# Performance work log

Measured on AMD Instinct MI355X. Metric: run time of the kernel, lower is better.

The kernel has to match this reference:

```python
import jax, jax.numpy as jnp
import numpy as np

B, T = 8, 32
D = 256                      # recurrent dim = 4*8*8 (product of embed dims)
SPEAKERS = 2
OUT_CELL = 64
N_CLASSES = 6
NUM_LAYERS = 2               # original shares ONE QRNNCell across layers ([cell]*num_layers)
BETA = 0.8                   # QActivation beta (scale_factor = 1)

def _unitary(rng, n):
    a = rng.normal(size=(n, n)) + 1j * rng.normal(size=(n, n))
    q, _ = np.linalg.qr(a)
    return jnp.asarray(q.real, jnp.float32), jnp.asarray(q.imag, jnp.float32)

def setup_inputs():
    key = jax.random.key(0)
    ks = jax.random.split(key, 18)
    rng = np.random.default_rng(0)
    def lin(k, fi, fo):
        kw, kb = jax.random.split(k)
        lim = 1.0 / np.sqrt(fi)
        return (jax.random.uniform(kw, (fi, fo), jnp.float32, -lim, lim),
                jax.random.uniform(kb, (fo,), jnp.float32, -lim, lim))
    Wt, bt = lin(ks[0], 300, 4)
    Wa, ba = lin(ks[1], 74, 8)
    Wv, bv = lin(ks[2], 35, 8)
    W1, b1 = lin(ks[3], D, OUT_CELL)
    W2, b2 = lin(ks[4], OUT_CELL, N_CLASSES)
    Ux_r, Ux_i = _unitary(rng, D)
    Uh_r, Uh_i = _unitary(rng, D)
    two_pi = float(2.0 * np.pi)
    return {
        'x_text': jax.random.normal(ks[5], (B, T, 300), jnp.float32),
        'x_audio': jax.random.normal(ks[6], (B, T, 74), jnp.float32),
        'x_video': jax.random.normal(ks[7], (B, T, 35), jnp.float32),
        'smask': jax.random.uniform(ks[8], (B, T, SPEAKERS), jnp.float32),
        'Wt': Wt, 'bt': bt, 'Wa': Wa, 'ba': ba, 'Wv': Wv, 'bv': bv,
        'Pt': jax.random.uniform(ks[9], (SPEAKERS, 4), jnp.float32, 0.0, two_pi),
        'Pa': jax.random.uniform(ks[10], (SPEAKERS, 8), jnp.float32, 0.0, two_pi),
        'Pv': jax.random.uniform(ks[11], (SPEAKERS, 8), jnp.float32, 0.0, two_pi),
        'Ux_r': Ux_r, 'Ux_i': Ux_i, 'Uh_r': Uh_r, 'Uh_i': Uh_i,
        'Lambda': jax.random.normal(ks[12], (), jnp.float32),
        'Kr': jax.random.normal(ks[13], (D, D), jnp.float32),
        'Ki': jax.random.normal(ks[14], (D, D), jnp.float32),
        'W1': W1, 'b1': b1, 'W2': W2, 'b2': b2,
    }

def _forward(x_text, x_audio, x_video, spk, Wt, bt, Wa, ba, Wv, bv, Pt, Pa, Pv,
             Ux_r, Ux_i, Uh_r, Uh_i, Lambda, Kr, Ki, W1, b1, W2, b2):
    def pure_state(x, W, b, P):
        r = jax.nn.relu(x @ W + b)
        amp = r / jnp.maximum(jnp.linalg.norm(r, axis=-1, keepdims=True), 1e-12)  # F.normalize
        ph = P[spk]                                   # (B,T,e) phase lookup by speaker id
        return amp * jnp.cos(ph), amp * jnp.sin(ph)   # ComplexMultiply
    tr_, ti_ = pure_state(x_text, Wt, bt, Pt)
    ar_, ai_ = pure_state(x_audio, Wa, ba, Pa)
    vr_, vi_ = pure_state(x_video, Wv, bv, Pv)
    def ckron(xr, xi, yr, yi):                        # QProduct: complex Kronecker product
        rr = jnp.einsum('bti,btj->btij', xr, yr) - jnp.einsum('bti,btj->btij', xi, yi)
        ii = jnp.einsum('bti,btj->btij', xr, yi) + jnp.einsum('bti,btj->btij', xi, yr)
        b_, t_ = rr.shape[:2]
        return rr.reshape(b_, t_, -1), ii.reshape(b_, t_, -1)
    pr, pi = ckron(tr_, ti_, ar_, ai_)
    pr, pi = ckron(pr, pi, vr_, vi_)                  # (B,T,D)
    # QOuter: rho = |psi><psi|, stored time-major for the scan
    rho_r = jnp.einsum('bti,btj->tbij', pr, pr) + jnp.einsum('bti,btj->tbij', pi, pi)
    rho_i = jnp.einsum('bti,btj->tbij', pi, pr) - jnp.einsum('bti,btj->tbij', pr, pi)
    lam = jax.nn.sigmoid(Lambda)
    eye = jnp.eye(D, dtype=pr.dtype) / D
    def evolve(Ur, Ui, rr, ri):                       # U rho U^dagger (complex, real/imag parts)
        Ar = jnp.einsum('pq,bqr->bpr', Ur, rr) - jnp.einsum('pq,bqr->bpr', Ui, ri)
        Ai = jnp.einsum('pq,bqr->bpr', Ur, ri) + jnp.einsum('pq,bqr->bpr', Ui, rr)
        Br = jnp.einsum('bpq,rq->bpr', Ar, Ur) + jnp.einsum('bpq,rq->bpr', Ai, Ui)
        Bi = jnp.einsum('bpq,rq->bpr', Ai, Ur) - jnp.einsum('bpq,rq->bpr', Ar, Ui)
        return Br, Bi
    def step(carry, x):                               # QRNNCell; activation only on emitted state
        hr, hi = carry
        xr, xi = x
        xer, xei = evolve(Ux_r, Ux_i, xr, xi)
        her, hei = evolve(Uh_r, Uh_i, hr, hi)
        nr = lam * xer + (1.0 - lam) * her
        ni = lam * xei + (1.0 - lam) * hei
        return (nr, ni), (BETA * nr + (1.0 - BETA) * eye, BETA * ni)  # QActivation (depolarize)
    xs = (rho_r, rho_i)
    for _ in range(NUM_LAYERS):                       # same (shared) cell each layer
        init = (jnp.broadcast_to(eye, rho_r.shape[1:]), jnp.zeros(rho_r.shape[1:], pr.dtype))
        _, xs = jax.lax.scan(step, init, xs)
    hr, hi = xs                                       # (T,B,D,D)
    # QMeasurement: p_k = Re <v_k| rho |v_k>, v_k L2-normalized complex vectors
    nrm = jnp.sqrt(jnp.sum(Kr * Kr + Ki * Ki, axis=-1, keepdims=True))
    mr, mi = Kr / nrm, Ki / nrm
    Prj_r = jnp.einsum('ki,kj->kij', mr, mr) + jnp.einsum('ki,kj->kij', mi, mi)
    Prj_i = jnp.einsum('ki,kj->kij', mr, mi) - jnp.einsum('ki,kj->kij', mi, mr)
    probs = jnp.einsum('tbij,kij->tbk', hr, Prj_r) - jnp.einsum('tbij,kij->tbk', hi, Prj_i)
    h1 = jax.nn.relu(probs @ W1 + b1)                 # SimpleNet (dropout = identity at eval)
    out = jnp.tanh(h1 @ W2 + b2)                      # (T,B,C)
    return jax.nn.log_softmax(jnp.moveaxis(out, 0, 1), axis=-1)  # (B,T,C)

def reference(x_text, x_audio, x_video, smask, Wt, bt, Wa, ba, Wv, bv, Pt, Pa, Pv,
              Ux_r, Ux_i, Uh_r, Uh_i, Lambda, Kr, Ki, W1, b1, W2, b2):
    spk = jnp.argmax(smask, axis=-1)
    return _forward(x_text, x_audio, x_video, spk, Wt, bt, Wa, ba, Wv, bv, Pt, Pa, Pv,
                    Ux_r, Ux_i, Uh_r, Uh_i, Lambda, Kr, Ki, W1, b1, W2, b2)
```

## Files before the change

### kernel.cpp

```cpp
#include <hip/hip_runtime.h>

#define TT 32
#define BETA_ 0.8f

typedef __bf16 bf16_t;
typedef bf16_t bf16x8 __attribute__((ext_vector_type(8)));
typedef float f32x4 __attribute__((ext_vector_type(4)));

#define PACC_F 256
#define BF_BASE_B 263168L
#define US4 262144L
#define XU  131072L
#define XIB_E (76L * US4)

__device__ inline f32x4 MF(bf16x8 a, bf16x8 b, f32x4 c) {
    return __builtin_amdgcn_mfma_f32_16x16x32_bf16(a, b, c, 0, 0, 0);
}

__device__ inline void splitW(float vr, float vi, bf16_t* o, long idx, int full) {
    bf16_t rh = (bf16_t)vr; o[idx] = rh;
    bf16_t ih = (bf16_t)vi; o[65536L + idx] = ih;
    if (full) {
        o[2 * 65536L + idx] = (bf16_t)(vr - (float)rh);
        o[3 * 65536L + idx] = (bf16_t)(vi - (float)ih);
    }
}

__global__ __launch_bounds__(256) void k_prep(
    const float* __restrict__ xt, const float* __restrict__ xa, const float* __restrict__ xv,
    const float* __restrict__ sm,
    const float* __restrict__ Wt, const float* __restrict__ bt,
    const float* __restrict__ Wa, const float* __restrict__ ba,
    const float* __restrict__ Wv, const float* __restrict__ bv,
    const float* __restrict__ Pt, const float* __restrict__ Pa, const float* __restrict__ Pv,
    const float* __restrict__ Uxr, const float* __restrict__ Uxi,
    const float* __restrict__ Uhr, const float* __restrict__ Uhi,
    const float* __restrict__ Lam, const float* __restrict__ Kr, const float* __restrict__ Ki,
    void* wsv)
{
    float* WF = (float*)wsv;
    bf16_t* bf = (bf16_t*)((char*)wsv + BF_BASE_B);
    const int blk = blockIdx.x, tid = threadIdx.x;
    __shared__ float red[256];
    __shared__ float rt[4], ra[8], rv[8], inv3[3];

    if (blk == 0) {
        if (tid != 0) return;
        float lam = 1.f / (1.f + expf(-Lam[0]));
        float oml = 1.f - lam;
        WF[0] = lam;
        WF[1] = BETA_ * BETA_ * lam * lam;
        float w = 1.f;
        for (int n = 0; n < 64; ++n) { WF[64 + n] = w; w *= oml; }
        float a1 = 1.f / 256.f, a2 = 1.f / 256.f;
        for (int t = 0; t < 32; ++t) {
            a1 = oml * a1;
            float y1 = BETA_ * a1 + (1.f - BETA_) / 256.f;
            a2 = lam * y1 + oml * a2;
            WF[8 + t] = BETA_ * a2 + (1.f - BETA_) / 256.f;
        }
        return;
    }
    if (blk < 513) {
        int i = (blk - 1) & 255, j = tid;
        if (blk < 257) {
            splitW(Uxr[i * 256 + j], Uxi[i * 256 + j], bf + 0 * US4, (long)i * 256 + j, 1);
        } else {
            float vr = Uhr[i * 256 + j], vi = Uhi[i * 256 + j];
            splitW(vr, vi, bf + 1 * US4, (long)i * 256 + j, 1);
            splitW(vr, vi, bf + 2 * US4, (long)j * 256 + i, 1);
        }
        return;
    }
    if (blk < 769) {
        const int colS = blk - 513;
        const int t0 = colS >> 3, b = colS & 7;
        const long bt_ = (long)b * TT + t0;
        if (tid < 4) {
            float acc = bt[tid];
            const float* x = xt + bt_ * 300;
            for (int q = 0; q < 300; ++q) acc = fmaf(x[q], Wt[q * 4 + tid], acc);
            rt[tid] = fmaxf(acc, 0.f);
        } else if (tid < 12) {
            int u = tid - 4;
            float acc = ba[u];
            const float* x = xa + bt_ * 74;
            for (int q = 0; q < 74; ++q) acc = fmaf(x[q], Wa[q * 8 + u], acc);
            ra[u] = fmaxf(acc, 0.f);
        } else if (tid < 20) {
            int u = tid - 12;
            float acc = bv[u];
            const float* x = xv + bt_ * 35;
            for (int q = 0; q < 35; ++q) acc = fmaf(x[q], Wv[q * 8 + u], acc);
            rv[u] = fmaxf(acc, 0.f);
        }
        __syncthreads();
        if (tid == 0) {
            float s = 0.f; for (int u = 0; u < 4; ++u) s += rt[u] * rt[u];
            inv3[0] = 1.f / fmaxf(sqrtf(s), 1e-12f);
            s = 0.f; for (int u = 0; u < 8; ++u) s += ra[u] * ra[u];
            inv3[1] = 1.f / fmaxf(sqrtf(s), 1e-12f);
            s = 0.f; for (int u = 0; u < 8; ++u) s += rv[u] * rv[u];
            inv3[2] = 1.f / fmaxf(sqrtf(s), 1e-12f);
        }
        __syncthreads();
        float s0 = sm[bt_ * 2], s1 = sm[bt_ * 2 + 1];
        int spk = (s1 > s0) ? 1 : 0;
        int d = tid;
        int ti = d >> 6, ai = (d >> 3) & 7, vi = d & 7;
        float amp = (rt[ti] * inv3[0]) * (ra[ai] * inv3[1]) * (rv[vi] * inv3[2]);
        float ph = Pt[spk * 4 + ti] + Pa[spk * 8 + ai] + Pv[spk * 8 + vi];
        splitW(amp * cosf(ph), amp * sinf(ph), bf + 3 * US4, (long)colS * 256 + d, 1);
        return;
    }
    {
        int k = blk - 769, i = tid;
        float vr = Kr[k * 256 + i], vi = Ki[k * 256 + i];
        red[i] = vr * vr + vi * vi;
        __syncthreads();
        for (int s = 128; s > 0; s >>= 1) { if (i < s) red[i] += red[i + s]; __syncthreads(); }
        float inv = 1.f / sqrtf(red[0]);
        splitW(vr * inv, -vi * inv, bf + 44 * US4, (long)k * 256 + i, 1);
    }
}

template<int LO, int WF>
__device__ void chain_body(const bf16_t* __restrict__ A, const bf16_t* __restrict__ B,
                           bf16_t* __restrict__ C,
                           int m0, int n0, int wm, int wn, int fr, int fg)
{
    constexpr int NP = LO ? 2 : 4;
    f32x4 rp[2][2] = {}, rn[2][2] = {}, im[2][2] = {};
    const bf16_t* Ab = A + (long)(m0 + wm * 32 + fr) * 256 + fg * 8;
    const bf16_t* Bb = B + (long)(n0 + wn * 32 + fr) * 256 + fg * 8;
#pragma unroll 2
    for (int ks = 0; ks < 8; ++ks) {
        bf16x8 aF[2][NP], bF[2][NP];
#pragma unroll
        for (int fm = 0; fm < 2; ++fm)
#pragma unroll
            for (int pl = 0; pl < NP; ++pl)
                aF[fm][pl] = *(const bf16x8*)(Ab + pl * 65536L + fm * 16 * 256L + ks * 32);
#pragma unroll
        for (int fn = 0; fn < 2; ++fn)
#pragma unroll
            for (int pl = 0; pl < NP; ++pl)
                bF[fn][pl] = *(const bf16x8*)(Bb + pl * 65536L + fn * 16 * 256L + ks * 32);
#pragma unroll
        for (int fm = 0; fm < 2; ++fm)
#pragma unroll
            for (int fn = 0; fn < 2; ++fn) {
                f32x4 p_ = rp[fm][fn], n_ = rn[fm][fn], i_ = im[fm][fn];
                p_ = MF(aF[fm][0], bF[fn][0], p_);
                n_ = MF(aF[fm][1], bF[fn][1], n_);
                i_ = MF(aF[fm][0], bF[fn][1], i_);
                i_ = MF(aF[fm][1], bF[fn][0], i_);
                if (!LO) {
                    p_ = MF(aF[fm][0], bF[fn][2], p_);
                    p_ = MF(aF[fm][2], bF[fn][0], p_);
                    n_ = MF(aF[fm][1], bF[fn][3], n_);
                    n_ = MF(aF[fm][3], bF[fn][1], n_);
                    i_ = MF(aF[fm][0], bF[fn][3], i_);
                    i_ = MF(aF[fm][2], bF[fn][1], i_);
                    i_ = MF(aF[fm][1], bF[fn][2], i_);
                    i_ = MF(aF[fm][3], bF[fn][0], i_);
                }
                rp[fm][fn] = p_; rn[fm][fn] = n_; im[fm][fn] = i_;
            }
    }
#pragma unroll
    for (int fm = 0; fm < 2; ++fm)
#pragma unroll
        for (int fn = 0; fn < 2; ++fn)
#pragma unroll
            for (int r4 = 0; r4 < 4; ++r4) {
                int m = m0 + wm * 32 + fm * 16 + fg * 4 + r4;
                int n = n0 + wn * 32 + fn * 16 + fr;
                float vr = rp[fm][fn][r4] - rn[fm][fn][r4];
                splitW(vr, im[fm][fn][r4], C, (long)m * 256 + n, WF);
            }
}

struct Jobs {
    long aB[4], aS[4], bB[4], cB[4], cS[4];
    int cnt[4], lo[4], wf[4];
};

__global__ __launch_bounds__(256) void k_chain(void* wsv, Jobs J)
{
    bf16_t* bf = (bf16_t*)((char*)wsv + BF_BASE_B);
    int z = blockIdx.y, j = 0;
    while (z >= J.cnt[j]) { z -= J.cnt[j]; ++j; }
    const bf16_t* A = bf + J.aB[j] + (long)z * J.aS[j];
    const bf16_t* B = bf + J.bB[j];
    bf16_t*       C = bf + J.cB[j] + (long)z * J.cS[j];
    const int m0 = (blockIdx.x & 3) * 64, n0 = (blockIdx.x >> 2) * 64;
    const int tid = threadIdx.x, lane = tid & 63, w = tid >> 6;
    const int wm = w >> 1, wn = w & 1, fr = lane & 15, fg = lane >> 4;
    if (J.lo[j])      chain_body<1, 0>(A, B, C, m0, n0, wm, wn, fr, fg);
    else if (J.wf[j]) chain_body<0, 1>(A, B, C, m0, n0, wm, wn, fr, fg);
    else              chain_body<0, 0>(A, B, C, m0, n0, wm, wn, fr, fg);
}

struct MJ { int pref[33]; };

__global__ __launch_bounds__(256) void k_measure6(void* wsv, MJ J)
{
    float* WF = (float*)wsv;
    bf16_t* bf = (bf16_t*)((char*)wsv + BF_BASE_B);
    int bid = blockIdx.x;
    int t = 0;
    while (bid >= J.pref[t + 1]) ++t;
    int jid = bid - J.pref[t];
    const int kblk = jid & 3;
    int g = jid >> 2;
    int i = 0;
    for (;;) { int cnt2 = ((t - 4 * i) >> 3) + 1; if (g < cnt2) break; g -= cnt2; ++i; }
    const int clo = 4 * i, colc = g;
    const int chi = (clo + 4 < t + 1) ? clo + 4 : t + 1;
    const int k0 = kblk * 64;

    const int tid = threadIdx.x, lane = tid & 63, w = tid >> 6;
    const int wm = w >> 1, wn = w & 1;
    const int fr = lane & 15, fg = lane >> 4;
    __shared__ float part[64][9];
    float sacc[2][2][4] = {};

    int t0_[2], bb_[2];
#pragma unroll
    for (int fn = 0; fn < 2; ++fn) {
        int g2 = wn * 32 + fn * 16 + fr;
        t0_[fn] = colc * 8 + (g2 >> 3);
        bb_[fn] = g2 & 7;
    }

    for (int c = clo; c < chi; ++c) {
        const bf16_t* Ab = bf + (44L + c) * US4 + (long)(k0 + wm * 32 + fr) * 256 + fg * 8;
        f32x4 rp[2][2] = {}, rn[2][2] = {}, im[2][2] = {};
        const bf16_t* Bb_[2];
        int val_[2];
#pragma unroll
        for (int fn = 0; fn < 2; ++fn) {
            int av = t - c - t0_[fn];
            val_[fn] = (av >= 0);
            Bb_[fn] = bf + XIB_E + (long)(val_[fn] ? av : 0) * XU
                    + (long)(t0_[fn] * 8 + bb_[fn]) * 256 + fg * 8;
        }
#pragma unroll 2
        for (int ks = 0; ks < 8; ++ks) {
            bf16x8 aF[2][2], bF[2][2];
#pragma unroll
            for (int fm = 0; fm < 2; ++fm)
#pragma unroll
                for (int pl = 0; pl < 2; ++pl)
                    aF[fm][pl] = *(const bf16x8*)(Ab + pl * 65536L + fm * 16 * 256L + ks * 32);
#pragma unroll
            for (int fn = 0; fn < 2; ++fn)
#pragma unroll
                for (int pl = 0; pl < 2; ++pl) {
                    bf16x8 v = bf16x8{};
                    if (val_[fn]) v = *(const bf16x8*)(Bb_[fn] + pl * 65536L + ks * 32);
                    bF[fn][pl] = v;
                }
#pragma unroll
            for (int fm = 0; fm < 2; ++fm)
#pragma unroll
                for (int fn = 0; fn < 2; ++fn) {
                    f32x4 p_ = rp[fm][fn], n_ = rn[fm][fn], i_ = im[fm][fn];
                    p_ = MF(aF[fm][0], bF[fn][0], p_);
                    n_ = MF(aF[fm][1], bF[fn][1], n_);
                    i_ = MF(aF[fm][0], bF[fn][1], i_);
                    i_ = MF(aF[fm][1], bF[fn][0], i_);
                    rp[fm][fn] = p_; rn[fm][fn] = n_; im[fm][fn] = i_;
                }
        }
#pragma unroll
        for (int fm = 0; fm < 2; ++fm)
#pragma unroll
            for (int fn = 0; fn < 2; ++fn)
#pragma unroll
                for (int r4 = 0; r4 < 4; ++r4) {
                    float vr = rp[fm][fn][r4] - rn[fm][fn][r4];
                    float vi = im[fm][fn][r4];
                    sacc[fm][fn][r4] += vr * vr + vi * vi;
                }
    }
    for (int e = tid; e < 64 * 9; e += 256) (&part[0][0])[e] = 0.f;
    __syncthreads();
#pragma unroll
    for (int fm = 0; fm < 2; ++fm)
#pragma unroll
        for (int fn = 0; fn < 2; ++fn)
#pragma unroll
            for (int r4 = 0; r4 < 4; ++r4) {
                int kl = wm * 32 + fm * 16 + fg * 4 + r4;
                if (t0_[fn] <= t)
                    atomicAdd(&part[kl][bb_[fn]], WF[64 + t - t0_[fn]] * sacc[fm][fn][r4]);
            }
    __syncthreads();
    float* pacc = WF + PACC_F;
    for (int e = tid; e < 512; e += 256) {
        int kl = e >> 3, b = e & 7;
        float v = part[kl][b];
        if (v != 0.f) atomicAdd(&pacc[((t * 8 + b) << 8) + k0 + kl], v);
    }
}

__global__ __launch_bounds__(64) void k_mlp(
    const float* __restrict__ W1, const float* __restrict__ b1,
    const float* __restrict__ W2, const float* __restrict__ b2,
    const float* __restrict__ WF, float* __restrict__ out)
{
    const int t = blockIdx.x >> 3, b = blockIdx.x & 7;
    const int tid = threadIdx.x;
    __shared__ float pp[256], hh[64], oo[6];
    float ft = WF[8 + t], s2 = WF[1];
    const float* pacc = WF + PACC_F + ((t * 8 + b) << 8);
    for (int k = tid; k < 256; k += 64) pp[k] = ft + s2 * pacc[k];
    __syncthreads();
    float acc = b1[tid];
    for (int k = 0; k < 256; ++k) acc = fmaf(pp[k], W1[k * 64 + tid], acc);
    hh[tid] = fmaxf(acc, 0.f);
    __syncthreads();
    if (tid < 6) {
        float a = b2[tid];
        for (int k = 0; k < 64; ++k) a = fmaf(hh[k], W2[k * 6 + tid], a);
        oo[tid] = tanhf(a);
    }
    __syncthreads();
    if (tid == 0) {
        float m = oo[0];
        for (int c2 = 1; c2 < 6; ++c2) m = fmaxf(m, oo[c2]);
        float s = 0.f;
        for (int c2 = 0; c2 < 6; ++c2) s += expf(oo[c2] - m);
        float lse = m + logf(s);
        for (int c2 = 0; c2 < 6; ++c2) out[((long)b * 32 + t) * 6 + c2] = oo[c2] - lse;
    }
}

static inline void setJob(Jobs& J, int i, long aB, long aS, long bB, long cB, long cS,
                          int cnt, int lo, int wf)
{
    J.aB[i] = aB; J.aS[i] = aS; J.bB[i] = bB; J.cB[i] = cB; J.cS[i] = cS;
    J.cnt[i] = cnt; J.lo[i] = lo; J.wf[i] = wf;
}

extern "C" void kernel_launch(void* const* d_in, const int* in_sizes, int n_in,
                              void* d_out, int out_size, void* d_ws, size_t ws_size,
                              hipStream_t stream)
{
    const float* xt  = (const float*)d_in[0];
    const float* xa  = (const float*)d_in[1];
    const float* xv  = (const float*)d_in[2];
    const float* sm  = (const float*)d_in[3];
    const float* Wt  = (const float*)d_in[4];
    const float* bt  = (const float*)d_in[5];
    const float* Wa  = (const float*)d_in[6];
    const float* ba  = (const float*)d_in[7];
    const float* Wv  = (const float*)d_in[8];
    const float* bv  = (const float*)d_in[9];
    const float* Pt  = (const float*)d_in[10];
    const float* Pa  = (const float*)d_in[11];
    const float* Pv  = (const float*)d_in[12];
    const float* Uxr = (const float*)d_in[13];
    const float* Uxi = (const float*)d_in[14];
    const float* Uhr = (const float*)d_in[15];
    const float* Uhi = (const float*)d_in[16];
    const float* Lam = (const float*)d_in[17];
    const float* Kr  = (const float*)d_in[18];
    const float* Ki  = (const float*)d_in[19];
    const float* W1  = (const float*)d_in[20];
    const float* b1  = (const float*)d_in[21];
    const float* W2  = (const float*)d_in[22];
    const float* b2  = (const float*)d_in[23];
    float* WF  = (float*)d_ws;
    float* out = (float*)d_out;

    hipMemsetAsync(WF + PACC_F, 0, 65536 * sizeof(float), stream);
    k_prep<<<1025, 256, 0, stream>>>(xt, xa, xv, sm, Wt, bt, Wa, ba, Wv, bv,
                                     Pt, Pa, Pv, Uxr, Uxi, Uhr, Uhi, Lam, Kr, Ki, d_ws);

    auto U = [](int u) { return (long)u * US4; };
    dim3 blk(256);
    Jobs J;

    setJob(J, 0, U(1), 0, U(2), U(4), 0, 1, 0, 1);
    setJob(J, 1, U(2), 0, U(1), U(5), 0, 1, 0, 1);
    setJob(J, 2, U(3), 0, U(0), U(12), 0, 1, 0, 1);
    setJob(J, 3, U(44), 0, U(2), U(45), 0, 1, 0, 1);
    k_chain<<<dim3(16, 4), blk, 0, stream>>>(d_ws, J);
    setJob(J, 0, U(4), 0, U(5), U(6), 0, 1, 0, 1);
    setJob(J, 1, U(5), 0, U(4), U(7), 0, 1, 0, 1);
    setJob(J, 2, U(12), 0, U(1), U(13), 0, 1, 0, 1);
    setJob(J, 3, U(44), US4, U(5), U(46), US4, 2, 0, 1);
    k_chain<<<dim3(16, 5), blk, 0, stream>>>(d_ws, J);
    setJob(J, 0, U(6), 0, U(7), U(8), 0, 1, 0, 1);
    setJob(J, 1, U(7), 0, U(6), U(9), 0, 1, 0, 1);
    setJob(J, 2, U(12), US4, U(4), U(14), US4, 2, 0, 1);
    setJob(J, 3, U(44), US4, U(7), U(48), US4, 4, 0, 1);
    k_chain<<<dim3(16, 8), blk, 0, stream>>>(d_ws, J);
    setJob(J, 0, U(8), 0, U(9), U(10), 0, 1, 0, 1);
    setJob(J, 1, U(9), 0, U(8), U(11), 0, 1, 0, 1);
    setJob(J, 2, U(12), US4, U(6), U(16), US4, 4, 0, 1);
    setJob(J, 3, U(44), US4, U(9), U(52), US4, 8, 0, 1);
    k_chain<<<dim3(16, 14), blk, 0, stream>>>(d_ws, J);
    setJob(J, 0, U(12), US4, U(8), U(20), US4, 8, 0, 1);
    setJob(J, 1, U(44), US4, U(11), U(60), US4, 16, 0, 0);
    setJob(J, 2, 0, 0, 0, 0, 0, 0, 0, 0);
    setJob(J, 3, 0, 0, 0, 0, 0, 0, 0, 0);
    k_chain<<<dim3(16, 24), blk, 0, stream>>>(d_ws, J);
    setJob(J, 0, U(12), US4, U(10), U(28), US4, 16, 0, 0);
    setJob(J, 1, U(12), US4, U(0), XIB_E, XU, 16, 1, 0);
    setJob(J, 2, 0, 0, 0, 0, 0, 0, 0, 0);
    setJob(J, 3, 0, 0, 0, 0, 0, 0, 0, 0);
    k_chain<<<dim3(16, 32), blk, 0, stream>>>(d_ws, J);
    setJob(J, 0, U(28), US4, U(0), XIB_E + 16 * XU, XU, 16, 1, 0);
    setJob(J, 1, 0, 0, 0, 0, 0, 0, 0, 0);
    setJob(J, 2, 0, 0, 0, 0, 0, 0, 0, 0);
    setJob(J, 3, 0, 0, 0, 0, 0, 0, 0, 0);
    k_chain<<<dim3(16, 16), blk, 0, stream>>>(d_ws, J);

    MJ mj;
    mj.pref[0] = 0;
    for (int t = 0; t < 32; ++t) {
        int G = 0;
        for (int i2 = 0; 4 * i2 <= t; ++i2) G += ((t - 4 * i2) >> 3) + 1;
        mj.pref[t + 1] = mj.pref[t] + G * 4;
    }
    k_measure6<<<dim3(mj.pref[32], 1, 1), blk, 0, stream>>>(d_ws, mj);
    k_mlp<<<256, 64, 0, stream>>>(W1, b1, W2, b2, WF, out);
}
```

Before: 424.3 us.

## Split measurement blocks per chain step, double-buffer MFMA loads, fold memset into prep

k_measure now gives each chain step c its own block instead of looping over up to 4 steps per block, so the grid has many more smaller blocks and each block does one register-tiled product before its atomic accumulation. Both chain and measure kernels use an explicit two-buffer software pipeline for global fragment loads ahead of the MFMAs, with occupancy hints added via launch_bounds. The hipMemsetAsync is replaced by extra k_prep blocks that zero the accumulator, removing one launch. In exchange, the finer split raises atomic traffic to global memory and duplicates A-fragment loads across blocks.

```diff
diff --git a/kernel.cpp b/kernel.cpp
--- a/kernel.cpp
+++ b/kernel.cpp
@@ -113,7 +113,7 @@
         splitW(amp * cosf(ph), amp * sinf(ph), bf + 3 * US4, (long)colS * 256 + d, 1);
         return;
     }
-    {
+    if (blk < 1025) {
         int k = blk - 769, i = tid;
         float vr = Kr[k * 256 + i], vi = Ki[k * 256 + i];
         red[i] = vr * vr + vi * vi;
@@ -121,53 +121,64 @@
         for (int s = 128; s > 0; s >>= 1) { if (i < s) red[i] += red[i + s]; __syncthreads(); }
         float inv = 1.f / sqrtf(red[0]);
         splitW(vr * inv, -vi * inv, bf + 44 * US4, (long)k * 256 + i, 1);
-    }
-}
-
-template<int LO, int WF>
-__device__ void chain_body(const bf16_t* __restrict__ A, const bf16_t* __restrict__ B,
-                           bf16_t* __restrict__ C,
-                           int m0, int n0, int wm, int wn, int fr, int fg)
+        return;
+    }
+    WF[PACC_F + (blk - 1025) * 256 + tid] = 0.f;
+}
+
+template<int LO, int WFull>
+__device__ __forceinline__ void chain_body(const bf16_t* __restrict__ A,
+                                           const bf16_t* __restrict__ B,
+                                           bf16_t* __restrict__ C,
+                                           int m0, int n0, int wm, int wn, int fr, int fg)
 {
     constexpr int NP = LO ? 2 : 4;
-    f32x4 rp[2][2] = {}, rn[2][2] = {}, im[2][2] = {};
     const bf16_t* Ab = A + (long)(m0 + wm * 32 + fr) * 256 + fg * 8;
     const bf16_t* Bb = B + (long)(n0 + wn * 32 + fr) * 256 + fg * 8;
-#pragma unroll 2
-    for (int ks = 0; ks < 8; ++ks) {
-        bf16x8 aF[2][NP], bF[2][NP];
-#pragma unroll
-        for (int fm = 0; fm < 2; ++fm)
-#pragma unroll
-            for (int pl = 0; pl < NP; ++pl)
-                aF[fm][pl] = *(const bf16x8*)(Ab + pl * 65536L + fm * 16 * 256L + ks * 32);
-#pragma unroll
-        for (int fn = 0; fn < 2; ++fn)
-#pragma unroll
-            for (int pl = 0; pl < NP; ++pl)
-                bF[fn][pl] = *(const bf16x8*)(Bb + pl * 65536L + fn * 16 * 256L + ks * 32);
-#pragma unroll
-        for (int fm = 0; fm < 2; ++fm)
-#pragma unroll
-            for (int fn = 0; fn < 2; ++fn) {
-                f32x4 p_ = rp[fm][fn], n_ = rn[fm][fn], i_ = im[fm][fn];
-                p_ = MF(aF[fm][0], bF[fn][0], p_);
-                n_ = MF(aF[fm][1], bF[fn][1], n_);
-                i_ = MF(aF[fm][0], bF[fn][1], i_);
-                i_ = MF(aF[fm][1], bF[fn][0], i_);
-                if (!LO) {
-                    p_ = MF(aF[fm][0], bF[fn][2], p_);
-                    p_ = MF(aF[fm][2], bF[fn][0], p_);
-                    n_ = MF(aF[fm][1], bF[fn][3], n_);
-                    n_ = MF(aF[fm][3], bF[fn][1], n_);
-                    i_ = MF(aF[fm][0], bF[fn][3], i_);
-                    i_ = MF(aF[fm][2], bF[fn][1], i_);
-                    i_ = MF(aF[fm][1], bF[fn][2], i_);
-                    i_ = MF(aF[fm][3], bF[fn][0], i_);
-                }
-                rp[fm][fn] = p_; rn[fm][fn] = n_; im[fm][fn] = i_;
-            }
-    }
+    f32x4 rp[2][2] = {}, rn[2][2] = {}, im[2][2] = {};
+    bf16x8 a0[2][NP], b0[2][NP], a1[2][NP], b1[2][NP];
+
+#define CLD(abuf, bbuf, ks)                                                            \
+    {                                                                                  \
+        _Pragma("unroll") for (int fm = 0; fm < 2; ++fm)                               \
+            _Pragma("unroll") for (int pl = 0; pl < NP; ++pl)                          \
+                abuf[fm][pl] = *(const bf16x8*)(Ab + pl * 65536L + fm * 4096L + (ks) * 32); \
+        _Pragma("unroll") for (int fn = 0; fn < 2; ++fn)                               \
+            _Pragma("unroll") for (int pl = 0; pl < NP; ++pl)                          \
+                bbuf[fn][pl] = *(const bf16x8*)(Bb + pl * 65536L + fn * 4096L + (ks) * 32); \
+    }
+#define CMM(abuf, bbuf)                                                                \
+    {                                                                                  \
+        _Pragma("unroll") for (int fm = 0; fm < 2; ++fm)                               \
+            _Pragma("unroll") for (int fn = 0; fn < 2; ++fn) {                         \
+                rp[fm][fn] = MF(abuf[fm][0], bbuf[fn][0], rp[fm][fn]);                 \
+                rn[fm][fn] = MF(abuf[fm][1], bbuf[fn][1], rn[fm][fn]);                 \
+                im[fm][fn] = MF(abuf[fm][0], bbuf[fn][1], im[fm][fn]);                 \
+                im[fm][fn] = MF(abuf[fm][1], bbuf[fn][0], im[fm][fn]);                 \
+                if (!LO) {                                                             \
+                    rp[fm][fn] = MF(abuf[fm][0], bbuf[fn][2], rp[fm][fn]);             \
+                    rp[fm][fn] = MF(abuf[fm][2], bbuf[fn][0], rp[fm][fn]);             \
+                    rn[fm][fn] = MF(abuf[fm][1], bbuf[fn][3], rn[fm][fn]);             \
+                    rn[fm][fn] = MF(abuf[fm][3], bbuf[fn][1], rn[fm][fn]);             \
+                    im[fm][fn] = MF(abuf[fm][0], bbuf[fn][3], im[fm][fn]);             \
+                    im[fm][fn] = MF(abuf[fm][2], bbuf[fn][1], im[fm][fn]);             \
+                    im[fm][fn] = MF(abuf[fm][1], bbuf[fn][2], im[fm][fn]);             \
+                    im[fm][fn] = MF(abuf[fm][3], bbuf[fn][0], im[fm][fn]);             \
+                }                                                                      \
+            }                                                                          \
+    }
+    CLD(a0, b0, 0);
+    CLD(a1, b1, 1);
+    CMM(a0, b0); CLD(a0, b0, 2);
+    CMM(a1, b1); CLD(a1, b1, 3);
+    CMM(a0, b0); CLD(a0, b0, 4);
+    CMM(a1, b1); CLD(a1, b1, 5);
+    CMM(a0, b0); CLD(a0, b0, 6);
+    CMM(a1, b1); CLD(a1, b1, 7);
+    CMM(a0, b0);
+    CMM(a1, b1);
+#undef CLD
+#undef CMM
 #pragma unroll
     for (int fm = 0; fm < 2; ++fm)
 #pragma unroll
@@ -177,7 +188,7 @@
                 int m = m0 + wm * 32 + fm * 16 + fg * 4 + r4;
                 int n = n0 + wn * 32 + fn * 16 + fr;
                 float vr = rp[fm][fn][r4] - rn[fm][fn][r4];
-                splitW(vr, im[fm][fn][r4], C, (long)m * 256 + n, WF);
+                splitW(vr, im[fm][fn][r4], C, (long)m * 256 + n, WFull);
             }
 }
 
@@ -186,7 +197,7 @@
     int cnt[4], lo[4], wf[4];
 };
 
-__global__ __launch_bounds__(256) void k_chain(void* wsv, Jobs J)
+__global__ __launch_bounds__(256, 2) void k_chain(void* wsv, Jobs J)
 {
     bf16_t* bf = (bf16_t*)((char*)wsv + BF_BASE_B);
     int z = blockIdx.y, j = 0;
@@ -204,7 +215,7 @@
 
 struct MJ { int pref[33]; };
 
-__global__ __launch_bounds__(256) void k_measure6(void* wsv, MJ J)
+__global__ __launch_bounds__(256, 3) void k_measure7(void* wsv, MJ J)
 {
     float* WF = (float*)wsv;
     bf16_t* bf = (bf16_t*)((char*)wsv + BF_BASE_B);
@@ -214,77 +225,66 @@
     int jid = bid - J.pref[t];
     const int kblk = jid & 3;
     int g = jid >> 2;
-    int i = 0;
-    for (;;) { int cnt2 = ((t - 4 * i) >> 3) + 1; if (g < cnt2) break; g -= cnt2; ++i; }
-    const int clo = 4 * i, colc = g;
-    const int chi = (clo + 4 < t + 1) ? clo + 4 : t + 1;
+    int c = 0;
+    for (;;) { int cnt2 = ((t - c) >> 3) + 1; if (g < cnt2) break; g -= cnt2; ++c; }
+    const int colc = g;
     const int k0 = kblk * 64;
 
     const int tid = threadIdx.x, lane = tid & 63, w = tid >> 6;
     const int wm = w >> 1, wn = w & 1;
     const int fr = lane & 15, fg = lane >> 4;
     __shared__ float part[64][9];
-    float sacc[2][2][4] = {};
-
-    int t0_[2], bb_[2];
+
+    int g2_[2], t0_[2], val_[2];
+    const bf16_t* Bb_[2];
 #pragma unroll
     for (int fn = 0; fn < 2; ++fn) {
-        int g2 = wn * 32 + fn * 16 + fr;
-        t0_[fn] = colc * 8 + (g2 >> 3);
-        bb_[fn] = g2 & 7;
-    }
-
-    for (int c = clo; c < chi; ++c) {
-        const bf16_t* Ab = bf + (44L + c) * US4 + (long)(k0 + wm * 32 + fr) * 256 + fg * 8;
-        f32x4 rp[2][2] = {}, rn[2][2] = {}, im[2][2] = {};
-        const bf16_t* Bb_[2];
-        int val_[2];
-#pragma unroll
-        for (int fn = 0; fn < 2; ++fn) {
-            int av = t - c - t0_[fn];
-            val_[fn] = (av >= 0);
-            Bb_[fn] = bf + XIB_E + (long)(val_[fn] ? av : 0) * XU
-                    + (long)(t0_[fn] * 8 + bb_[fn]) * 256 + fg * 8;
-        }
-#pragma unroll 2
-        for (int ks = 0; ks < 8; ++ks) {
-            bf16x8 aF[2][2], bF[2][2];
-#pragma unroll
-            for (int fm = 0; fm < 2; ++fm)
-#pragma unroll
-                for (int pl = 0; pl < 2; ++pl)
-                    aF[fm][pl] = *(const bf16x8*)(Ab + pl * 65536L + fm * 16 * 256L + ks * 32);
-#pragma unroll
-            for (int fn = 0; fn < 2; ++fn)
-#pragma unroll
-                for (int pl = 0; pl < 2; ++pl) {
-                    bf16x8 v = bf16x8{};
-                    if (val_[fn]) v = *(const bf16x8*)(Bb_[fn] + pl * 65536L + ks * 32);
-                    bF[fn][pl] = v;
-                }
-#pragma unroll
-            for (int fm = 0; fm < 2; ++fm)
-#pragma unroll
-                for (int fn = 0; fn < 2; ++fn) {
-                    f32x4 p_ = rp[fm][fn], n_ = rn[fm][fn], i_ = im[fm][fn];
-                    p_ = MF(aF[fm][0], bF[fn][0], p_);
-                    n_ = MF(aF[fm][1], bF[fn][1], n_);
-                    i_ = MF(aF[fm][0], bF[fn][1], i_);
-                    i_ = MF(aF[fm][1], bF[fn][0], i_);
-                    rp[fm][fn] = p_; rn[fm][fn] = n_; im[fm][fn] = i_;
-                }
-        }
-#pragma unroll
-        for (int fm = 0; fm < 2; ++fm)
-#pragma unroll
-            for (int fn = 0; fn < 2; ++fn)
-#pragma unroll
-                for (int r4 = 0; r4 < 4; ++r4) {
-                    float vr = rp[fm][fn][r4] - rn[fm][fn][r4];
-                    float vi = im[fm][fn][r4];
-                    sacc[fm][fn][r4] += vr * vr + vi * vi;
-                }
-    }
+        g2_[fn] = colc * 64 + wn * 32 + fn * 16 + fr;
+        t0_[fn] = g2_[fn] >> 3;
+        int av = t - c - t0_[fn];
+        val_[fn] = (av >= 0);
+        Bb_[fn] = bf + XIB_E + (long)(val_[fn] ? av : 0) * XU + (long)g2_[fn] * 256 + fg * 8;
+    }
+    const bf16_t* Ab = bf + (44L + c) * US4 + (long)(k0 + wm * 32 + fr) * 256 + fg * 8;
+
+    f32x4 rp[2][2] = {}, rn[2][2] = {}, im[2][2] = {};
+    bf16x8 a0[2][2], b0[2][2], a1[2][2], b1[2][2];
+
+#define MLD(abuf, bbuf, ks)                                                            \
+    {                                                                                  \
+        _Pragma("unroll") for (int fm = 0; fm < 2; ++fm)                               \
+            _Pragma("unroll") for (int pl = 0; pl < 2; ++pl)                           \
+                abuf[fm][pl] = *(const bf16x8*)(Ab + pl * 65536L + fm * 4096L + (ks) * 32); \
+        _Pragma("unroll") for (int fn = 0; fn < 2; ++fn)                               \
+            _Pragma("unroll") for (int pl = 0; pl < 2; ++pl) {                         \
+                bf16x8 v = bf16x8{};                                                   \
+                if (val_[fn]) v = *(const bf16x8*)(Bb_[fn] + pl * 65536L + (ks) * 32); \
+                bbuf[fn][pl] = v;                                                      \
+            }                                                                          \
+    }
+#define MMM(abuf, bbuf)                                                                \
+    {                                                                                  \
+        _Pragma("unroll") for (int fm = 0; fm < 2; ++fm)                               \
+            _Pragma("unroll") for (int fn = 0; fn < 2; ++fn) {                         \
+                rp[fm][fn] = MF(abuf[fm][0], bbuf[fn][0], rp[fm][fn]);                 \
+                rn[fm][fn] = MF(abuf[fm][1], bbuf[fn][1], rn[fm][fn]);                 \
+                im[fm][fn] = MF(abuf[fm][0], bbuf[fn][1], im[fm][fn]);                 \
+                im[fm][fn] = MF(abuf[fm][1], bbuf[fn][0], im[fm][fn]);                 \
+            }                                                                          \
+    }
+    MLD(a0, b0, 0);
+    MLD(a1, b1, 1);
+    MMM(a0, b0); MLD(a0, b0, 2);
+    MMM(a1, b1); MLD(a1, b1, 3);
+    MMM(a0, b0); MLD(a0, b0, 4);
+    MMM(a1, b1); MLD(a1, b1, 5);
+    MMM(a0, b0); MLD(a0, b0, 6);
+    MMM(a1, b1); MLD(a1, b1, 7);
+    MMM(a0, b0);
+    MMM(a1, b1);
+#undef MLD
+#undef MMM
+
     for (int e = tid; e < 64 * 9; e += 256) (&part[0][0])[e] = 0.f;
     __syncthreads();
 #pragma unroll
@@ -293,9 +293,12 @@
         for (int fn = 0; fn < 2; ++fn)
 #pragma unroll
             for (int r4 = 0; r4 < 4; ++r4) {
+                float vr = rp[fm][fn][r4] - rn[fm][fn][r4];
+                float vi = im[fm][fn][r4];
+                float v = vr * vr + vi * vi;
                 int kl = wm * 32 + fm * 16 + fg * 4 + r4;
-                if (t0_[fn] <= t)
-                    atomicAdd(&part[kl][bb_[fn]], WF[64 + t - t0_[fn]] * sacc[fm][fn][r4]);
+                if (val_[fn] && t0_[fn] <= t)
+                    atomicAdd(&part[kl][g2_[fn] & 7], WF[64 + t - t0_[fn]] * v);
             }
     __syncthreads();
     float* pacc = WF + PACC_F;
@@ -376,8 +379,7 @@
     float* WF  = (float*)d_ws;
     float* out = (float*)d_out;
 
-    hipMemsetAsync(WF + PACC_F, 0, 65536 * sizeof(float), stream);
-    k_prep<<<1025, 256, 0, stream>>>(xt, xa, xv, sm, Wt, bt, Wa, ba, Wv, bv,
+    k_prep<<<1281, 256, 0, stream>>>(xt, xa, xv, sm, Wt, bt, Wa, ba, Wv, bv,
                                      Pt, Pa, Pv, Uxr, Uxi, Uhr, Uhi, Lam, Kr, Ki, d_ws);
 
     auto U = [](int u) { return (long)u * US4; };
@@ -424,9 +426,9 @@
     mj.pref[0] = 0;
     for (int t = 0; t < 32; ++t) {
         int G = 0;
-        for (int i2 = 0; 4 * i2 <= t; ++i2) G += ((t - 4 * i2) >> 3) + 1;
+        for (int c = 0; c <= t; ++c) G += ((t - c) >> 3) + 1;
         mj.pref[t + 1] = mj.pref[t] + G * 4;
     }
-    k_measure6<<<dim3(mj.pref[32], 1, 1), blk, 0, stream>>>(d_ws, mj);
+    k_measure7<<<dim3(mj.pref[32], 1, 1), blk, 0, stream>>>(d_ws, mj);
     k_mlp<<<256, 64, 0, stream>>>(W1, b1, W2, b2, WF, out);
 }
```

New measurement: 386.9 us. -8.8%, faster.
